# Optimization experiments

Hardware: AMD Instinct MI355X
Metric: run time of the kernel (lower is better)

## Reference

```python
import jax, jax.numpy as jnp
import numpy as np

B, T, C, H = 4, 2048, 1024, 16
D = C // H  # head_dim = 64
ROPE_BASE = 10000.0


def _rope_cos_sin(T, D, dtype):
    # inv_freq: (D/2,), freqs: (T, D/2) -> cos/sin tiled to (T, D)
    inv_freq = 1.0 / (ROPE_BASE ** (jnp.arange(0, D, 2, dtype=jnp.float32) / D))
    freqs = jnp.arange(T, dtype=jnp.float32)[:, None] * inv_freq[None, :]
    emb = jnp.concatenate([freqs, freqs], axis=-1)  # (T, D)
    return jnp.cos(emb).astype(dtype), jnp.sin(emb).astype(dtype)


def _rotate_half(x):
    x1, x2 = jnp.split(x, 2, axis=-1)
    return jnp.concatenate([-x2, x1], axis=-1)


def setup_inputs() -> dict:
    key = jax.random.key(0)
    k1, k2, k3 = jax.random.split(key, 3)
    x = jax.random.normal(k1, (B, T, C), dtype=jnp.float32)
    W_qkv = jax.random.normal(k2, (C, 3 * C), dtype=jnp.float32) * (C ** -0.5)
    b_qkv = jnp.zeros((3 * C,), dtype=jnp.float32)
    W_out = jax.random.normal(k3, (C, C), dtype=jnp.float32) * (C ** -0.5)
    b_out = jnp.zeros((C,), dtype=jnp.float32)
    return {"x": x, "W_qkv": W_qkv, "b_qkv": b_qkv, "W_out": W_out, "b_out": b_out}


def reference(x, W_qkv, b_qkv, W_out, b_out):
    Bx, Tx, Cx = x.shape
    qkv = x @ W_qkv + b_qkv                                   # (B, T, 3C)
    qkv = qkv.reshape(Bx, Tx, 3, H, D).transpose(2, 0, 3, 1, 4)  # (3, B, H, T, D)
    q, k, v = qkv[0], qkv[1], qkv[2]

    cos, sin = _rope_cos_sin(Tx, D, x.dtype)                  # (T, D) each
    q = q * cos + _rotate_half(q) * sin
    k = k * cos + _rotate_half(k) * sin

    # NOTE: original code has no 1/sqrt(D) scaling — faithful reproduction.
    att = jnp.einsum('bhtd,bhsd->bhts', q, k)                 # (B, H, T, T)
    causal = jnp.tril(jnp.ones((Tx, Tx), dtype=bool))
    att = jnp.where(causal[None, None, :, :], att, -jnp.inf)
    att = jax.nn.softmax(att, axis=-1)
    y = jnp.einsum('bhts,bhsd->bhtd', att, v)                 # (B, H, T, D)
    y = y.transpose(0, 2, 1, 3).reshape(Bx, Tx, Cx)
    return y @ W_out + b_out
```

## Files before the change

### kernel.cpp

```cpp
#include <hip/hip_runtime.h>
#include <math.h>

#define NB    4
#define T_SEQ 2048
#define CDIM  1024
#define NH    16
#define DH    64
#define NQKV  3072

typedef short bf16x8 __attribute__((ext_vector_type(8)));
typedef float f32x4  __attribute__((ext_vector_type(4)));

#define GLOBAL_AS __attribute__((address_space(1)))
#define LDS_AS    __attribute__((address_space(3)))

__device__ __forceinline__ void async16(const void* g, void* l) {
  __builtin_amdgcn_global_load_lds((const GLOBAL_AS void*)g, (LDS_AS void*)l, 16, 0, 0);
}

__device__ __forceinline__ unsigned short f2bf(float f) {
  unsigned u = __float_as_uint(f);
  unsigned r = u + 0x7FFF + ((u >> 16) & 1);
  return (unsigned short)(r >> 16);
}

#define SWZ8(row, c) ((((row) << 3) | ((c) ^ ((row) & 7))) << 3)

#define BARRIER()  asm volatile("s_barrier" ::: "memory")
#define VMCNT(n)   asm volatile("s_waitcnt vmcnt(" #n ")" ::: "memory")

__global__ __launch_bounds__(256) void convert_bf16(
    const float* __restrict__ in, unsigned short* __restrict__ out, int n4) {
  int i = blockIdx.x * 256 + threadIdx.x;
  if (i >= n4) return;
  float4 v = ((const float4*)in)[i];
  ushort4 o;
  o.x = f2bf(v.x); o.y = f2bf(v.y); o.z = f2bf(v.z); o.w = f2bf(v.w);
  ((ushort4*)out)[i] = o;
}

__global__ __launch_bounds__(256) void transpose_to_bf16(
    const float* __restrict__ in, unsigned short* __restrict__ out, int K, int N) {
  __shared__ float tile[32][33];
  int n0 = blockIdx.x << 5, k0 = blockIdx.y << 5;
  int r  = threadIdx.x >> 3;
  int c4 = (threadIdx.x & 7) << 2;
  float4 v = *(const float4*)&in[(size_t)(k0 + r) * N + n0 + c4];
  tile[r][c4 + 0] = v.x; tile[r][c4 + 1] = v.y;
  tile[r][c4 + 2] = v.z; tile[r][c4 + 3] = v.w;
  __syncthreads();
  ushort4 o;
  o.x = f2bf(tile[c4 + 0][r]); o.y = f2bf(tile[c4 + 1][r]);
  o.z = f2bf(tile[c4 + 2][r]); o.w = f2bf(tile[c4 + 3][r]);
  *(ushort4*)&out[(size_t)(n0 + r) * K + k0 + c4] = o;
}

__global__ __launch_bounds__(256) void transpose_v(
    const unsigned short* __restrict__ v, unsigned short* __restrict__ vt) {
  __shared__ unsigned short tile[64][65];
  int bh = blockIdx.y;
  int t0 = blockIdx.x << 6;
  size_t ib = (size_t)bh * (T_SEQ * DH);
  int tid = threadIdx.x;
#pragma unroll
  for (int u = 0; u < 2; ++u) {
    int f = u * 256 + tid;
    int tr = f >> 3, c = f & 7;
    bf16x8 val = *(const bf16x8*)&v[ib + (size_t)(t0 + tr) * DH + c * 8];
#pragma unroll
    for (int j = 0; j < 8; ++j) tile[tr][c * 8 + j] = (unsigned short)val[j];
  }
  __syncthreads();
#pragma unroll
  for (int u = 0; u < 2; ++u) {
    int f = u * 256 + tid;
    int d = f >> 3, c = f & 7;
    bf16x8 o;
#pragma unroll
    for (int j = 0; j < 8; ++j) o[j] = (short)tile[c * 8 + j][d];
    *(bf16x8*)&vt[ib + (size_t)d * T_SEQ + t0 + c * 8] = o;
  }
}

#define GEMM_PIPE(Aptr, Btptr)                                                \
  __shared__ short As[2][128 * 64];                                           \
  __shared__ short Bs[2][256 * 64];                                           \
  int m0 = blockIdx.y << 7, n0 = blockIdx.x << 8;                             \
  int tid = threadIdx.x;                                                      \
  int wave = tid >> 6, lane = tid & 63;                                       \
  int wm = wave >> 2, wn = wave & 3;                                          \
  int col = lane & 15, quad = lane >> 4;                                      \
  int srow = tid >> 3;                                                        \
  int schunk = (tid & 7) ^ (srow & 7);                                        \
  const unsigned short* aSrc = &Aptr[(size_t)(m0 + srow) * CDIM + schunk * 8];\
  const unsigned short* bSrc = &Btptr[(size_t)(n0 + srow) * CDIM + schunk * 8];\
  int d0 = wave * 512;  \
  f32x4 acc[4][4];                                                            \
  _Pragma("unroll") for (int mt = 0; mt < 4; ++mt)                            \
  _Pragma("unroll") for (int nt = 0; nt < 4; ++nt)                            \
    acc[mt][nt] = (f32x4){0.f, 0.f, 0.f, 0.f};                                \
    \
  async16(aSrc,          &As[0][d0]);                                         \
  async16(aSrc + 65536,  &As[0][d0 + 4096]);                                  \
  async16(bSrc,          &Bs[0][d0]);                                         \
  async16(bSrc + 65536,  &Bs[0][d0 + 4096]);                                  \
  async16(bSrc + 131072, &Bs[0][d0 + 8192]);                                  \
  async16(bSrc + 196608, &Bs[0][d0 + 12288]);                                 \
  for (int kt = 0; kt < 16; ++kt) {                                           \
    int p = kt & 1;                                                           \
    if (kt < 15) {                                                            \
      const unsigned short* a_ = aSrc + (kt + 1) * 64;                        \
      const unsigned short* b_ = bSrc + (kt + 1) * 64;                        \
      async16(a_,          &As[p ^ 1][d0]);                                   \
      async16(a_ + 65536,  &As[p ^ 1][d0 + 4096]);                            \
      async16(b_,          &Bs[p ^ 1][d0]);                                   \
      async16(b_ + 65536,  &Bs[p ^ 1][d0 + 4096]);                            \
      async16(b_ + 131072, &Bs[p ^ 1][d0 + 8192]);                            \
      async16(b_ + 196608, &Bs[p ^ 1][d0 + 12288]);                           \
      VMCNT(6);          \
    } else {                                                                  \
      VMCNT(0);                                         \
    }                                                                         \
    BARRIER();                           \
    _Pragma("unroll") for (int ks = 0; ks < 2; ++ks) {                        \
      bf16x8 af[4], bfr[4];                                                   \
      _Pragma("unroll") for (int mt = 0; mt < 4; ++mt)                        \
        af[mt] = *(const bf16x8*)&As[p][SWZ8(wm * 64 + mt * 16 + col,         \
                                             ks * 4 + quad)];                 \
      _Pragma("unroll") for (int nt = 0; nt < 4; ++nt)                        \
        bfr[nt] = *(const bf16x8*)&Bs[p][SWZ8(wn * 64 + nt * 16 + col,        \
                                              ks * 4 + quad)];                \
      BARRIER();                                                              \
      __builtin_amdgcn_s_setprio(1);                                          \
      _Pragma("unroll") for (int mt = 0; mt < 4; ++mt)                        \
        _Pragma("unroll") for (int nt = 0; nt < 4; ++nt)                      \
          acc[mt][nt] = __builtin_amdgcn_mfma_f32_16x16x32_bf16(              \
              af[mt], bfr[nt], acc[mt][nt], 0, 0, 0);                         \
      __builtin_amdgcn_s_setprio(0);                                          \
      BARRIER();                                                              \
    }                                                                         \
  }

__global__ __launch_bounds__(512, 2) void gemm_qkv_mfma(
    const unsigned short* __restrict__ A, const unsigned short* __restrict__ Bt,
    const float* __restrict__ bias,
    unsigned short* __restrict__ qb, unsigned short* __restrict__ kb,
    unsigned short* __restrict__ vb) {
  GEMM_PIPE(A, Bt)
  int nn = n0 + wn * 64;
  int which = nn >> 10;
  int h = (nn >> 6) & 15;
  unsigned short* dst = (which == 0) ? qb : ((which == 1) ? kb : vb);
  float bv[4];
#pragma unroll
  for (int nt = 0; nt < 4; ++nt) bv[nt] = bias[nn + nt * 16 + col];
  if (which < 2) {
    float invf0 = expf((float)col * -0.28782313662425572f);
    float invf1 = expf((float)(col + 16) * -0.28782313662425572f);
#pragma unroll
    for (int mt = 0; mt < 4; ++mt) {
#pragma unroll
      for (int r = 0; r < 4; ++r) {
        int m = m0 + wm * 64 + mt * 16 + quad * 4 + r;
        int bidx = m >> 11, t = m & 2047;
        float x0 = acc[mt][0][r] + bv[0];
        float x1 = acc[mt][1][r] + bv[1];
        float x2 = acc[mt][2][r] + bv[2];
        float x3 = acc[mt][3][r] + bv[3];
        float s0a, c0a, s1a, c1a;
        sincosf((float)t * invf0, &s0a, &c0a);
        sincosf((float)t * invf1, &s1a, &c1a);
        size_t ro = (((size_t)bidx * NH + h) * T_SEQ + t) * DH;
        dst[ro + col]      = f2bf(x0 * c0a - x2 * s0a);
        dst[ro + col + 16] = f2bf(x1 * c1a - x3 * s1a);
        dst[ro + col + 32] = f2bf(x2 * c0a + x0 * s0a);
        dst[ro + col + 48] = f2bf(x3 * c1a + x1 * s1a);
      }
    }
  } else {
#pragma unroll
    for (int mt = 0; mt < 4; ++mt) {
#pragma unroll
      for (int r = 0; r < 4; ++r) {
        int m = m0 + wm * 64 + mt * 16 + quad * 4 + r;
        int bidx = m >> 11, t = m & 2047;
        size_t ro = (((size_t)bidx * NH + h) * T_SEQ + t) * DH;
        dst[ro + col]      = f2bf(acc[mt][0][r] + bv[0]);
        dst[ro + col + 16] = f2bf(acc[mt][1][r] + bv[1]);
        dst[ro + col + 32] = f2bf(acc[mt][2][r] + bv[2]);
        dst[ro + col + 48] = f2bf(acc[mt][3][r] + bv[3]);
      }
    }
  }
}

__global__ __launch_bounds__(512, 2) void gemm_out_mfma(
    const unsigned short* __restrict__ A, const unsigned short* __restrict__ Bt,
    const float* __restrict__ bias, float* __restrict__ out) {
  GEMM_PIPE(A, Bt)
#pragma unroll
  for (int nt = 0; nt < 4; ++nt) {
    int n = n0 + wn * 64 + nt * 16 + col;
    float bv = bias[n];
#pragma unroll
    for (int mt = 0; mt < 4; ++mt) {
#pragma unroll
      for (int r = 0; r < 4; ++r) {
        int m = m0 + wm * 64 + mt * 16 + quad * 4 + r;
        out[(size_t)m * CDIM + n] = acc[mt][nt][r] + bv;
      }
    }
  }
}

__global__ __launch_bounds__(256) void attn_mfma(
    const unsigned short* __restrict__ qg, const unsigned short* __restrict__ kg,
    const unsigned short* __restrict__ vtg, unsigned short* __restrict__ yb) {
  __shared__ short Qs[128 * 64];
  __shared__ short Ks[64 * 64];
  __shared__ short Vts[64 * 64];
  __shared__ short Ps[4][32][72];
  int tid = threadIdx.x;
  int wave = tid >> 6, lane = tid & 63;
  int col = lane & 15, quad = lane >> 4;
  int bh = blockIdx.x;
  int qblk = 15 - (int)blockIdx.y;
  int qb0 = qblk << 7;
  size_t base = (size_t)bh * (T_SEQ * DH);

#pragma unroll
  for (int u = 0; u < 4; ++u) {
    int ff = u * 256 + wave * 64 + lane;
    int row = ff >> 3, cl = ff & 7;
    int cg = cl ^ (row & 7);
    async16(&qg[base + (size_t)(qb0 + row) * DH + cg * 8],
            &Qs[(u * 256 + wave * 64) * 8]);
  }

  bf16x8 ones;
#pragma unroll
  for (int j = 0; j < 8; ++j) ones[j] = (short)0x3F80;

  f32x4 oc[2][4], lsum[2];
#pragma unroll
  for (int mf = 0; mf < 2; ++mf) {
    lsum[mf] = (f32x4){0.f, 0.f, 0.f, 0.f};
#pragma unroll
    for (int dt = 0; dt < 4; ++dt) oc[mf][dt] = (f32x4){0.f, 0.f, 0.f, 0.f};
  }

  int qlo = qb0 + wave * 32;
  int qhi = qlo + 31;
  int nkb = (qblk << 1) + 2;
  for (int kb = 0; kb < nkb; ++kb) {
    int s0 = kb << 6;
    __syncthreads();
#pragma unroll
    for (int u = 0; u < 2; ++u) {
      int ff = u * 256 + wave * 64 + lane;
      int row = ff >> 3, cl = ff & 7;
      int cg = cl ^ (row & 7);
      async16(&kg[base + (size_t)(s0 + row) * DH + cg * 8],
              &Ks[(u * 256 + wave * 64) * 8]);
      async16(&vtg[base + (size_t)row * T_SEQ + s0 + cg * 8],
              &Vts[(u * 256 + wave * 64) * 8]);
    }
    __syncthreads();
    if (s0 > qhi) continue;

    f32x4 sc[2][4];
#pragma unroll
    for (int mf = 0; mf < 2; ++mf)
#pragma unroll
      for (int nt = 0; nt < 4; ++nt) sc[mf][nt] = (f32x4){0.f, 0.f, 0.f, 0.f};
#pragma unroll
    for (int kc = 0; kc < 2; ++kc) {
      bf16x8 aq0 = *(const bf16x8*)&Qs[SWZ8(wave * 32 + col,      kc * 4 + quad)];
      bf16x8 aq1 = *(const bf16x8*)&Qs[SWZ8(wave * 32 + 16 + col, kc * 4 + quad)];
#pragma unroll
      for (int nt = 0; nt < 4; ++nt) {
        bf16x8 bk = *(const bf16x8*)&Ks[SWZ8(nt * 16 + col, kc * 4 + quad)];
        sc[0][nt] = __builtin_amdgcn_mfma_f32_16x16x32_bf16(aq0, bk, sc[0][nt], 0, 0, 0);
        sc[1][nt] = __builtin_amdgcn_mfma_f32_16x16x32_bf16(aq1, bk, sc[1][nt], 0, 0, 0);
      }
    }

    if (s0 + 63 > qlo) {
#pragma unroll
      for (int mf = 0; mf < 2; ++mf)
#pragma unroll
        for (int nt = 0; nt < 4; ++nt) {
          int s_glob = s0 + nt * 16 + col;
#pragma unroll
          for (int r = 0; r < 4; ++r)
            if (s_glob > qlo + mf * 16 + quad * 4 + r) sc[mf][nt][r] = -3.0e38f;
        }
    }

#pragma unroll
    for (int mf = 0; mf < 2; ++mf)
#pragma unroll
      for (int nt = 0; nt < 4; ++nt)
#pragma unroll
        for (int r = 0; r < 4; ++r)
          Ps[wave][mf * 16 + quad * 4 + r][nt * 16 + col] =
              (short)f2bf(__expf(sc[mf][nt][r]));

#pragma unroll
    for (int kc = 0; kc < 2; ++kc) {
      bf16x8 ap0 = *(const bf16x8*)&Ps[wave][col][kc * 32 + quad * 8];
      bf16x8 ap1 = *(const bf16x8*)&Ps[wave][16 + col][kc * 32 + quad * 8];
      lsum[0] = __builtin_amdgcn_mfma_f32_16x16x32_bf16(ap0, ones, lsum[0], 0, 0, 0);
      lsum[1] = __builtin_amdgcn_mfma_f32_16x16x32_bf16(ap1, ones, lsum[1], 0, 0, 0);
#pragma unroll
      for (int dt = 0; dt < 4; ++dt) {
        bf16x8 vb = *(const bf16x8*)&Vts[SWZ8(dt * 16 + col, kc * 4 + quad)];
        oc[0][dt] = __builtin_amdgcn_mfma_f32_16x16x32_bf16(ap0, vb, oc[0][dt], 0, 0, 0);
        oc[1][dt] = __builtin_amdgcn_mfma_f32_16x16x32_bf16(ap1, vb, oc[1][dt], 0, 0, 0);
      }
    }
  }

  int b = bh >> 4, h = bh & 15;
#pragma unroll
  for (int mf = 0; mf < 2; ++mf)
#pragma unroll
    for (int dt = 0; dt < 4; ++dt) {
      int d = dt * 16 + col;
#pragma unroll
      for (int r = 0; r < 4; ++r) {
        int t = qb0 + wave * 32 + mf * 16 + quad * 4 + r;
        yb[(((size_t)b * T_SEQ + t) * NH + h) * DH + d] =
            f2bf(oc[mf][dt][r] / lsum[mf][r]);
      }
    }
}

extern "C" void kernel_launch(void* const* d_in, const int* in_sizes, int n_in,
                              void* d_out, int out_size, void* d_ws, size_t ws_size,
                              hipStream_t stream) {
  const float* x     = (const float*)d_in[0];
  const float* W_qkv = (const float*)d_in[1];
  const float* b_qkv = (const float*)d_in[2];
  const float* W_out = (const float*)d_in[3];
  const float* b_out = (const float*)d_in[4];
  float* out = (float*)d_out;

  const size_t per = (size_t)NB * NH * T_SEQ * DH;
  unsigned short* xb  = (unsigned short*)d_ws;
  unsigned short* qb  = xb + per;
  unsigned short* kbf = qb + per;
  unsigned short* vbf = kbf + per;
  unsigned short* vtb = vbf + per;
  unsigned short* yb  = vtb + per;
  unsigned short* wqt = yb + per;
  unsigned short* wot = wqt + (size_t)NQKV * CDIM;

  convert_bf16<<<(int)(per / 4 / 256), 256, 0, stream>>>(x, xb, (int)(per / 4));
  transpose_to_bf16<<<dim3(NQKV / 32, CDIM / 32), 256, 0, stream>>>(W_qkv, wqt, CDIM, NQKV);
  transpose_to_bf16<<<dim3(CDIM / 32, CDIM / 32), 256, 0, stream>>>(W_out, wot, CDIM, CDIM);
  gemm_qkv_mfma<<<dim3(NQKV / 256, (NB * T_SEQ) / 128), 512, 0, stream>>>(
      xb, wqt, b_qkv, qb, kbf, vbf);
  transpose_v<<<dim3(T_SEQ / 64, NB * NH), 256, 0, stream>>>(vbf, vtb);
  attn_mfma<<<dim3(NB * NH, T_SEQ / 128), 256, 0, stream>>>(qb, kbf, vtb, yb);
  gemm_out_mfma<<<dim3(CDIM / 256, (NB * T_SEQ) / 128), 512, 0, stream>>>(
      yb, wot, b_out, out);
}
```

Measured before the change: 286.8 us.

## Triple-buffer GEMM K-loop with one barrier per tile and precompute RoPE table

The shared GEMM pipeline moves from double to triple LDS buffering. Loads are issued two K-tiles ahead, and the two per-substep barriers are dropped, leaving a single barrier per tile. This cuts synchronisation stalls and lets memory loads overlap more compute in both projection GEMMs. Separately, a small kernel builds a cos/sin table so the QKV epilogue reads it instead of calling expf/sincosf per element. The costs are more LDS per block (144KB) and one extra kernel launch plus table reads.

```diff
diff --git a/kernel.cpp b/kernel.cpp
--- a/kernel.cpp
+++ b/kernel.cpp
@@ -28,6 +28,15 @@
 
 #define BARRIER()  asm volatile("s_barrier" ::: "memory")
 #define VMCNT(n)   asm volatile("s_waitcnt vmcnt(" #n ")" ::: "memory")
+
+__global__ __launch_bounds__(256) void rope_table(float2* __restrict__ tab) {
+  int i = blockIdx.x * 256 + threadIdx.x;
+  int t = i >> 5, d = i & 31;
+  float inv = expf((float)d * -0.28782313662425572f);
+  float s, c;
+  sincosf((float)t * inv, &s, &c);
+  tab[i] = make_float2(c, s);
+}
 
 __global__ __launch_bounds__(256) void convert_bf16(
     const float* __restrict__ in, unsigned short* __restrict__ out, int n4) {
@@ -82,9 +91,19 @@
   }
 }
 
+#define STAGE(kt, b)                                                          \
+  { const unsigned short* sa_ = aSrc + (kt) * 64;                             \
+    const unsigned short* sb_ = bSrc + (kt) * 64;                             \
+    async16(sa_,          &As[b][d0]);                                        \
+    async16(sa_ + 65536,  &As[b][d0 + 4096]);                                 \
+    async16(sb_,          &Bs[b][d0]);                                        \
+    async16(sb_ + 65536,  &Bs[b][d0 + 4096]);                                 \
+    async16(sb_ + 131072, &Bs[b][d0 + 8192]);                                 \
+    async16(sb_ + 196608, &Bs[b][d0 + 12288]); }
+
 #define GEMM_PIPE(Aptr, Btptr)                                                \
-  __shared__ short As[2][128 * 64];                                           \
-  __shared__ short Bs[2][256 * 64];                                           \
+  __shared__ short As[3][128 * 64];                                           \
+  __shared__ short Bs[3][256 * 64];                                           \
   int m0 = blockIdx.y << 7, n0 = blockIdx.x << 8;                             \
   int tid = threadIdx.x;                                                      \
   int wave = tid >> 6, lane = tid & 63;                                       \
@@ -94,56 +113,40 @@
   int schunk = (tid & 7) ^ (srow & 7);                                        \
   const unsigned short* aSrc = &Aptr[(size_t)(m0 + srow) * CDIM + schunk * 8];\
   const unsigned short* bSrc = &Btptr[(size_t)(n0 + srow) * CDIM + schunk * 8];\
-  int d0 = wave * 512;  \
+  int d0 = wave * 512;      \
   f32x4 acc[4][4];                                                            \
   _Pragma("unroll") for (int mt = 0; mt < 4; ++mt)                            \
   _Pragma("unroll") for (int nt = 0; nt < 4; ++nt)                            \
     acc[mt][nt] = (f32x4){0.f, 0.f, 0.f, 0.f};                                \
-    \
-  async16(aSrc,          &As[0][d0]);                                         \
-  async16(aSrc + 65536,  &As[0][d0 + 4096]);                                  \
-  async16(bSrc,          &Bs[0][d0]);                                         \
-  async16(bSrc + 65536,  &Bs[0][d0 + 4096]);                                  \
-  async16(bSrc + 131072, &Bs[0][d0 + 8192]);                                  \
-  async16(bSrc + 196608, &Bs[0][d0 + 12288]);                                 \
-  for (int kt = 0; kt < 16; ++kt) {                                           \
-    int p = kt & 1;                                                           \
-    if (kt < 15) {                                                            \
-      const unsigned short* a_ = aSrc + (kt + 1) * 64;                        \
-      const unsigned short* b_ = bSrc + (kt + 1) * 64;                        \
-      async16(a_,          &As[p ^ 1][d0]);                                   \
-      async16(a_ + 65536,  &As[p ^ 1][d0 + 4096]);                            \
-      async16(b_,          &Bs[p ^ 1][d0]);                                   \
-      async16(b_ + 65536,  &Bs[p ^ 1][d0 + 4096]);                            \
-      async16(b_ + 131072, &Bs[p ^ 1][d0 + 8192]);                            \
-      async16(b_ + 196608, &Bs[p ^ 1][d0 + 12288]);                           \
-      VMCNT(6);          \
-    } else {                                                                  \
-      VMCNT(0);                                         \
-    }                                                                         \
-    BARRIER();                           \
+  STAGE(0, 0)                                                                 \
+  STAGE(1, 1)                                                                 \
+  _Pragma("unroll")                                                           \
+  for (int t = 0; t < 16; ++t) {                                              \
+    if (t < 15) { VMCNT(6); } else { VMCNT(0); }                              \
+    BARRIER();                                                                \
+    if (t + 2 < 16) STAGE(t + 2, (t + 2) % 3)                                 \
+    const short* A_ = As[t % 3];                                              \
+    const short* B_ = Bs[t % 3];                                              \
     _Pragma("unroll") for (int ks = 0; ks < 2; ++ks) {                        \
       bf16x8 af[4], bfr[4];                                                   \
       _Pragma("unroll") for (int mt = 0; mt < 4; ++mt)                        \
-        af[mt] = *(const bf16x8*)&As[p][SWZ8(wm * 64 + mt * 16 + col,         \
-                                             ks * 4 + quad)];                 \
+        af[mt] = *(const bf16x8*)&A_[SWZ8(wm * 64 + mt * 16 + col,            \
+                                          ks * 4 + quad)];                    \
       _Pragma("unroll") for (int nt = 0; nt < 4; ++nt)                        \
-        bfr[nt] = *(const bf16x8*)&Bs[p][SWZ8(wn * 64 + nt * 16 + col,        \
-                                              ks * 4 + quad)];                \
-      BARRIER();                                                              \
+        bfr[nt] = *(const bf16x8*)&B_[SWZ8(wn * 64 + nt * 16 + col,           \
+                                           ks * 4 + quad)];                   \
       __builtin_amdgcn_s_setprio(1);                                          \
       _Pragma("unroll") for (int mt = 0; mt < 4; ++mt)                        \
         _Pragma("unroll") for (int nt = 0; nt < 4; ++nt)                      \
           acc[mt][nt] = __builtin_amdgcn_mfma_f32_16x16x32_bf16(              \
               af[mt], bfr[nt], acc[mt][nt], 0, 0, 0);                         \
       __builtin_amdgcn_s_setprio(0);                                          \
-      BARRIER();                                                              \
     }                                                                         \
   }
 
 __global__ __launch_bounds__(512, 2) void gemm_qkv_mfma(
     const unsigned short* __restrict__ A, const unsigned short* __restrict__ Bt,
-    const float* __restrict__ bias,
+    const float* __restrict__ bias, const float2* __restrict__ rope,
     unsigned short* __restrict__ qb, unsigned short* __restrict__ kb,
     unsigned short* __restrict__ vb) {
   GEMM_PIPE(A, Bt)
@@ -155,8 +158,6 @@
 #pragma unroll
   for (int nt = 0; nt < 4; ++nt) bv[nt] = bias[nn + nt * 16 + col];
   if (which < 2) {
-    float invf0 = expf((float)col * -0.28782313662425572f);
-    float invf1 = expf((float)(col + 16) * -0.28782313662425572f);
 #pragma unroll
     for (int mt = 0; mt < 4; ++mt) {
 #pragma unroll
@@ -167,14 +168,13 @@
         float x1 = acc[mt][1][r] + bv[1];
         float x2 = acc[mt][2][r] + bv[2];
         float x3 = acc[mt][3][r] + bv[3];
-        float s0a, c0a, s1a, c1a;
-        sincosf((float)t * invf0, &s0a, &c0a);
-        sincosf((float)t * invf1, &s1a, &c1a);
+        float2 cs0 = rope[(t << 5) + col];
+        float2 cs1 = rope[(t << 5) + col + 16];
         size_t ro = (((size_t)bidx * NH + h) * T_SEQ + t) * DH;
-        dst[ro + col]      = f2bf(x0 * c0a - x2 * s0a);
-        dst[ro + col + 16] = f2bf(x1 * c1a - x3 * s1a);
-        dst[ro + col + 32] = f2bf(x2 * c0a + x0 * s0a);
-        dst[ro + col + 48] = f2bf(x3 * c1a + x1 * s1a);
+        dst[ro + col]      = f2bf(x0 * cs0.x - x2 * cs0.y);
+        dst[ro + col + 16] = f2bf(x1 * cs1.x - x3 * cs1.y);
+        dst[ro + col + 32] = f2bf(x2 * cs0.x + x0 * cs0.y);
+        dst[ro + col + 48] = f2bf(x3 * cs1.x + x1 * cs1.y);
       }
     }
   } else {
@@ -355,12 +355,14 @@
   unsigned short* yb  = vtb + per;
   unsigned short* wqt = yb + per;
   unsigned short* wot = wqt + (size_t)NQKV * CDIM;
-
+  float2* rope = (float2*)(wot + (size_t)CDIM * CDIM);
+
+  rope_table<<<256, 256, 0, stream>>>(rope);
   convert_bf16<<<(int)(per / 4 / 256), 256, 0, stream>>>(x, xb, (int)(per / 4));
   transpose_to_bf16<<<dim3(NQKV / 32, CDIM / 32), 256, 0, stream>>>(W_qkv, wqt, CDIM, NQKV);
   transpose_to_bf16<<<dim3(CDIM / 32, CDIM / 32), 256, 0, stream>>>(W_out, wot, CDIM, CDIM);
   gemm_qkv_mfma<<<dim3(NQKV / 256, (NB * T_SEQ) / 128), 512, 0, stream>>>(
-      xb, wqt, b_qkv, qb, kbf, vbf);
+      xb, wqt, b_qkv, rope, qb, kbf, vbf);
   transpose_v<<<dim3(T_SEQ / 64, NB * NH), 256, 0, stream>>>(vbf, vtb);
   attn_mfma<<<dim3(NB * NH, T_SEQ / 128), 256, 0, stream>>>(qb, kbf, vtb, yb);
   gemm_out_mfma<<<dim3(CDIM / 256, (NB * T_SEQ) / 128), 512, 0, stream>>>(
```

Measured after the change: 261.7 us. 8.8% less time.
